# Performance work log

Measured on AMD Instinct MI355X. Metric: run time of the kernel, lower is better.

Reference implementation:

```python
import jax, jax.numpy as jnp
import numpy as np

MAX_N = 21
COORD = 3
TOTAL_T = 100
K_RANK = 3
POWER_STEPS = 10


def _recon_single(D, Wt, u_noise, x_noise):
    """D, Wt: [N,N]; u_noise: [K_RANK,N]; x_noise: [N,3]. Returns X: [N,3]."""
    N = MAX_N
    # dist_to_gram (classical MDS double-centering)
    D_row = jnp.sum(D, 0, keepdims=True) / N
    D_col = jnp.sum(D, 1, keepdims=True) / N
    D_mean = jnp.sum(D) / (N * N)
    B = -0.5 * (D - D_row - D_col + D_mean)
    # low_rank_approx_power: k=3 deflated power iterations, 10 steps each
    A = B
    us = []
    for i in range(K_RANK):
        u = u_noise[i]
        for _ in range(POWER_STEPS):
            # F.normalize(u, dim=0, p=2, eps=0.001)
            u = u / jnp.maximum(jnp.linalg.norm(u), 1e-3)
            u = A @ u
        eig_sq = jnp.sum(u * u)
        u = u / jnp.power(eig_sq + 0.01, 0.25)
        us.append(u)
        A = A - jnp.outer(u, u)
    X0 = jnp.stack(us, -1) + x_noise  # [N,3]

    T = jnp.float32(TOTAL_T)

    def energy(X):
        diff = X[None, :, :] - X[:, None, :]          # [N,N,3], D_X[i,j]=||X_j-X_i||^2
        D_X = jnp.sum(diff * diff, -1) + 0.01
        return jnp.sum(Wt * jnp.square(D - D_X))

    def step(X, t):
        g = jax.grad(energy)(X)
        dX = -0.1 * g
        speed = jnp.sqrt(jnp.sum(dX * dX, 1, keepdims=True) + 1e-3)
        alpha_t = 0.1 + (5.0 - 0.1) * ((T - t) / T)
        scale = alpha_t * jnp.tanh(speed / alpha_t) / speed
        return X + dX * scale, None

    X, _ = jax.lax.scan(step, X0, jnp.arange(TOTAL_T, dtype=jnp.float32))
    return X


def _forward(gnn_edge_out, W1, b1, W2, b2, u_noise, x_noise, batch_size):
    h_nf = W1.shape[1]
    # edge_mlp1 (MLP with 1 layer -> Linear + ReLU)
    edge_out = jax.nn.relu(gnn_edge_out @ W1 + b1)                     # [B*N*N, h]
    emb = jnp.sum(edge_out.reshape(batch_size, MAX_N, MAX_N, h_nf), axis=(1, 2))  # [B, h]
    # edge_mlp2 -> symmetrize -> softplus
    e2 = (edge_out @ W2 + b2).reshape(batch_size, MAX_N, MAX_N, 2)
    e2 = e2 + jnp.transpose(e2, (0, 2, 1, 3))
    dw = jax.nn.softplus(e2)
    D_init = dw[..., 0] * (1.0 - jnp.eye(MAX_N, dtype=dw.dtype))       # [B,N,N]
    W = dw[..., 1]                                                     # [B,N,N]
    X_pred = jax.vmap(_recon_single)(D_init, W, u_noise, x_noise)      # [B,N,3]
    return D_init, W, emb, X_pred


def setup_inputs() -> dict:
    key = jax.random.key(0)
    ks = jax.random.split(key, 5)
    B, h_nf = 1024, 256
    n_edges = B * MAX_N * MAX_N
    return {
        "gnn_edge_out": jax.random.normal(ks[0], (n_edges, h_nf), jnp.float32),
        "W1": jax.random.normal(ks[1], (h_nf, h_nf), jnp.float32) * (1.0 / np.sqrt(h_nf)),
        "b1": jnp.zeros((h_nf,), jnp.float32),
        "W2": jax.random.normal(ks[2], (h_nf, 2), jnp.float32) * (1.0 / np.sqrt(h_nf)),
        "b2": jnp.zeros((2,), jnp.float32),
        "u_noise": jax.random.normal(ks[3], (B, K_RANK, MAX_N), jnp.float32),
        "x_noise": jax.random.normal(ks[4], (B, MAX_N, COORD), jnp.float32),
        "batch_size": B,
    }


def reference(gnn_edge_out, W1, b1, W2, b2, u_noise, x_noise, batch_size):
    return _forward(gnn_edge_out, W1, b1, W2, b2, u_noise, x_noise, batch_size)
```

## Files before the change

kernel.cpp:

```cpp
#include <hip/hip_runtime.h>
#include <hip/hip_bf16.h>
#include <math.h>

#define B_SZ 1024
#define NMAX 21
#define NN 441
#define HNF 256
#define TOT_ROWS (B_SZ * NN)
#define TILES_PER_BATCH 7
#define BMV 63

typedef short short8 __attribute__((ext_vector_type(8)));
typedef float float4v __attribute__((ext_vector_type(4)));

__device__ __forceinline__ unsigned short f2bf(float x) {
    union { float f; unsigned int u; } v; v.f = x;
    unsigned int r = v.u + 0x7FFFu + ((v.u >> 16) & 1u);
    return (unsigned short)(r >> 16);
}

__device__ __forceinline__ unsigned pk_bf16(float lo, float hi) {
    __hip_bfloat162 h = __float22bfloat162_rn(float2{lo, hi});
    return *reinterpret_cast<unsigned*>(&h);
}

__device__ __forceinline__ float softplus_fast(float x) {
    float e = __builtin_amdgcn_exp2f(-fabsf(x) * 1.44269504088896f);
    float lg = __builtin_amdgcn_logf(1.f + e);
    return fmaxf(x, 0.f) + 0.69314718055995f * lg;
}

__device__ __forceinline__ float tanh_fast(float x) {
    float e = __builtin_amdgcn_exp2f(x * 2.8853900817779268f);
    float q = __builtin_amdgcn_rcpf(e + 1.f);
    return fmaf(-2.f, q, 1.f);
}

__global__ __launch_bounds__(256) void pack_w1(const float* __restrict__ W1,
                                               short* __restrict__ B0p,
                                               float* __restrict__ emb)
{
    int id = blockIdx.x * 256 + threadIdx.x;
    int j = id & 7, l = (id >> 3) & 63, f = (id >> 9) & 15, s = id >> 13;
    int k = s * 32 + ((l >> 4) << 3) + j;
    int c = (f << 4) + (l & 15);
    B0p[id] = (short)f2bf(W1[k * HNF + c]);
    #pragma unroll
    for (int e = 0; e < 4; e++)
        emb[(size_t)e * 65536 + id] = 0.f;
}

__global__ __launch_bounds__(512, 4) void fused_mlp_bf16(
    const float* __restrict__ gnn, const short* __restrict__ B0p,
    const float* __restrict__ b1, const float* __restrict__ W2,
    const float* __restrict__ b2,
    float* __restrict__ Dreg, float* __restrict__ Wreg, float* __restrict__ emb)
{
    __shared__ __align__(16) char ldsbuf[65536];
    float* stage = (float*)ldsbuf;
    short* Abf   = (short*)ldsbuf;
    __shared__ float red0[8][64];
    __shared__ float red1[8][64];

    const int t = threadIdx.x;
    const int w = t >> 6, l = t & 63;
    const int batch = blockIdx.x / TILES_PER_BATCH;
    const int tile  = blockIdx.x % TILES_PER_BATCH;
    const long row0 = (long)batch * NN + (long)tile * BMV;

    #pragma unroll
    for (int i = 0; i < 8; i++) {
        int r = (w << 3) + i;
        long ar = row0 + r;
        if (ar >= (long)TOT_ROWS) ar = TOT_ROWS - 1;
        const float* gsrc = gnn + ar * HNF + (l << 2);
        __builtin_amdgcn_global_load_lds(
            (const __attribute__((address_space(1))) unsigned*)gsrc,
            (__attribute__((address_space(3))) unsigned*)(stage + (r << 8)),
            16, 0, 0);
    }
    asm volatile("s_waitcnt vmcnt(0)" ::: "memory");

    const int kk_s = l >> 3;
    const int fk_s = (l >> 1) & 3;
    const int jh_s = l & 1;
    uint2 pv[8];
    #pragma unroll
    for (int i = 0; i < 8; i++) {
        int r = (w << 3) + i;
        float4 f = *(const float4*)(stage + (r << 8) + (l << 2));
        pv[i].x = pk_bf16(f.x, f.y);
        pv[i].y = pk_bf16(f.z, f.w);
    }
    __syncthreads();
    #pragma unroll
    for (int i = 0; i < 8; i++) {
        int r = (w << 3) + i;
        int di = (((kk_s << 2) + (r >> 4)) << 6) | (fk_s << 4) | (r & 15);
        *(uint2*)(Abf + (((size_t)(di ^ kk_s)) << 3) + (jh_s << 2)) = pv[i];
    }
    __syncthreads();

    const int frow = l & 15;
    const int fk   = l >> 4;

    float4v acc[4][2];
    #pragma unroll
    for (int m = 0; m < 4; m++)
        #pragma unroll
        for (int n = 0; n < 2; n++)
            acc[m][n] = (float4v){0.f, 0.f, 0.f, 0.f};

    #pragma unroll 2
    for (int kk = 0; kk < 8; ++kk) {
        short8 bf[2], af[4];
        #pragma unroll
        for (int n = 0; n < 2; n++) {
            int nf = (w << 1) + n;
            size_t off = (size_t)((((kk << 4) + nf) << 6) | l) << 3;
            bf[n] = *(const short8*)(B0p + off);
        }
        #pragma unroll
        for (int m = 0; m < 4; m++) {
            int di = ((((kk << 2) + m) << 6) | l) ^ kk;
            af[m] = *(const short8*)(Abf + (size_t)di * 8);
        }
        #pragma unroll
        for (int m = 0; m < 4; m++)
            #pragma unroll
            for (int n = 0; n < 2; n++)
                acc[m][n] = __builtin_amdgcn_mfma_f32_16x16x32_bf16(af[m], bf[n], acc[m][n], 0, 0, 0);
    }

    float w20[2], w21[2], b1v[2];
    #pragma unroll
    for (int n = 0; n < 2; n++) {
        int cc = (((w << 1) + n) << 4) + frow;
        b1v[n] = b1[cc];
        w20[n] = W2[2 * cc];
        w21[n] = W2[2 * cc + 1];
    }
    float ps0[4][4], ps1[4][4], embp[2] = {0.f, 0.f};
    #pragma unroll
    for (int m = 0; m < 4; m++)
        #pragma unroll
        for (int j = 0; j < 4; j++) { ps0[m][j] = 0.f; ps1[m][j] = 0.f; }

    #pragma unroll
    for (int m = 0; m < 4; m++)
        #pragma unroll
        for (int n = 0; n < 2; n++)
            #pragma unroll
            for (int j = 0; j < 4; j++) {
                float h = fmaxf(acc[m][n][j] + b1v[n], 0.f);
                ps0[m][j] += h * w20[n];
                ps1[m][j] += h * w21[n];
                int row = (m << 4) + (fk << 2) + j;
                if (row < BMV) embp[n] += h;
            }

    #pragma unroll
    for (int off = 1; off < 16; off <<= 1)
        #pragma unroll
        for (int m = 0; m < 4; m++)
            #pragma unroll
            for (int j = 0; j < 4; j++) {
                ps0[m][j] += __shfl_xor(ps0[m][j], off);
                ps1[m][j] += __shfl_xor(ps1[m][j], off);
            }
    if (frow == 0) {
        #pragma unroll
        for (int m = 0; m < 4; m++)
            #pragma unroll
            for (int j = 0; j < 4; j++) {
                int row = (m << 4) + (fk << 2) + j;
                red0[w][row] = ps0[m][j];
                red1[w][row] = ps1[m][j];
            }
    }

    #pragma unroll
    for (int n = 0; n < 2; n++) {
        embp[n] += __shfl_xor(embp[n], 16);
        embp[n] += __shfl_xor(embp[n], 32);
    }
    if (l < 16) {
        #pragma unroll
        for (int n = 0; n < 2; n++)
            atomicAdd(emb + (size_t)batch * 256 + (((w << 1) + n) << 4) + l, embp[n]);
    }

    __syncthreads();
    if (t < BMV) {
        float v0 = b2[0], v1 = b2[1];
        #pragma unroll
        for (int ww = 0; ww < 8; ww++) { v0 += red0[ww][t]; v1 += red1[ww][t]; }
        Dreg[row0 + t] = v0;
        Wreg[row0 + t] = v1;
    }
}

__global__ __launch_bounds__(64) void symrecon_kernel(
    float* __restrict__ Dreg, float* __restrict__ Wreg,
    const float* __restrict__ un, const float* __restrict__ xn,
    float* __restrict__ Xo)
{
    const int b = blockIdx.x, l = threadIdx.x;
    __shared__ float R0[NN], R1[NN];
    __shared__ float Rs[22], Us[22], Xs[3][22];

    float* Db = Dreg + (size_t)b * NN;
    float* Wb = Wreg + (size_t)b * NN;
    for (int idx = l; idx < NN; idx += 64) { R0[idx] = Db[idx]; R1[idx] = Wb[idx]; }
    if (l == 0) { Rs[21] = 0.f; Us[21] = 0.f; Xs[0][21] = 0.f; Xs[1][21] = 0.f; Xs[2][21] = 0.f; }
    __syncthreads();

    const int half = l >> 5;
    const int li   = l & 31;
    const bool act = li < NMAX;
    const int li0  = act ? li : 0;
    const int q0   = half * 11;

    float Drow[11], Wrow[11], WD[11];
    float rsh = 0.f;
    #pragma unroll
    for (int j = 0; j < 11; j++) {
        int q = q0 + j;
        bool v = act && (q < NMAX);
        int qc = v ? q : 0;
        float rd = R0[li0 * NMAX + qc] + R0[qc * NMAX + li0];
        float rw = R1[li0 * NMAX + qc] + R1[qc * NMAX + li0];
        float d  = (v && q != li) ? softplus_fast(rd) : 0.f;
        float wv = v ? softplus_fast(rw) : 0.f;
        Drow[j] = d; Wrow[j] = wv; WD[j] = wv * d;
        rsh += d;
    }
    if (act) {
        #pragma unroll
        for (int j = 0; j < 11; j++) {
            int q = q0 + j;
            if (q < NMAX) {
                Db[li * NMAX + q] = Drow[j];
                Wb[li * NMAX + q] = Wrow[j];
            }
        }
    }

    float rsf = rsh + __shfl_xor(rsh, 32);
    float tot = rsh;
    #pragma unroll
    for (int m = 1; m < 64; m <<= 1) tot += __shfl_xor(tot, m);
    const float mean = tot * (1.f / (float)NN);
    const float rsn  = rsf * (1.f / (float)NMAX);
    if (act && half == 0) Rs[li] = rsn;
    float Arow[11];
    #pragma unroll
    for (int j = 0; j < 11; j++) {
        int q = q0 + j;
        bool v = act && (q < NMAX);
        float rsq = Rs[q];
        Arow[j] = v ? -0.5f * (Drow[j] - rsn - rsq + mean) : 0.f;
    }

    float xc[3];
    #pragma unroll
    for (int e = 0; e < 3; e++) {
        float u = act ? un[(size_t)b * 63 + e * NMAX + li] : 0.f;
        for (int s = 0; s < 10; s++) {
            float n2 = (act && half == 0) ? u * u : 0.f;
            #pragma unroll
            for (int m = 1; m < 64; m <<= 1) n2 += __shfl_xor(n2, m);
            u *= fminf(__builtin_amdgcn_rsqf(n2), 1000.f);
            if (act && half == 0) Us[li] = u;
            float a = 0.f;
            #pragma unroll
            for (int j = 0; j < 11; j++) a = fmaf(Arow[j], Us[q0 + j], a);
            a += __shfl_xor(a, 32);
            u = act ? a : 0.f;
        }
        float e2 = (act && half == 0) ? u * u : 0.f;
        #pragma unroll
        for (int m = 1; m < 64; m <<= 1) e2 += __shfl_xor(e2, m);
        u *= sqrtf(__builtin_amdgcn_rsqf(e2 + 0.01f));
        xc[e] = u;
        if (act && half == 0) Us[li] = u;
        #pragma unroll
        for (int j = 0; j < 11; j++) Arow[j] = fmaf(-u, Us[q0 + j], Arow[j]);
    }
    float x = xc[0], y = xc[1], z = xc[2];
    if (act) {
        x += xn[(size_t)b * 63 + li * 3 + 0];
        y += xn[(size_t)b * 63 + li * 3 + 1];
        z += xn[(size_t)b * 63 + li * 3 + 2];
    }
    if (act && half == 0) { Xs[0][li] = x; Xs[1][li] = y; Xs[2][li] = z; }

    for (int tstep = 0; tstep < 100; tstep++) {
        float gx = 0.f, gy = 0.f, gz = 0.f;
        #pragma unroll
        for (int j = 0; j < 11; j++) {
            int q = q0 + j;
            float dx = x - Xs[0][q];
            float dy = y - Xs[1][q];
            float dz = z - Xs[2][q];
            float s  = fmaf(dx, dx, fmaf(dy, dy, fmaf(dz, dz, 0.01f)));
            float cm = fmaf(-Wrow[j], s, WD[j]);
            gx = fmaf(cm, dx, gx);
            gy = fmaf(cm, dy, gy);
            gz = fmaf(cm, dz, gz);
        }
        gx += __shfl_xor(gx, 32);
        gy += __shfl_xor(gy, 32);
        gz += __shfl_xor(gz, 32);
        float d0 = 0.8f * gx, d1 = 0.8f * gy, d2 = 0.8f * gz;
        float ss = fmaf(d0, d0, fmaf(d1, d1, fmaf(d2, d2, 1e-3f)));
        float inv_sp = __builtin_amdgcn_rsqf(ss);
        float speed  = ss * inv_sp;
        float alpha  = fmaf(-0.049f, (float)tstep, 5.0f);
        float th     = tanh_fast(speed * __builtin_amdgcn_rcpf(alpha));
        float scale  = alpha * th * inv_sp;
        x = fmaf(d0, scale, x);
        y = fmaf(d1, scale, y);
        z = fmaf(d2, scale, z);
        if (act && half == 0) { Xs[0][li] = x; Xs[1][li] = y; Xs[2][li] = z; }
    }
    if (act && half == 0) {
        Xo[(size_t)b * 63 + li * 3 + 0] = x;
        Xo[(size_t)b * 63 + li * 3 + 1] = y;
        Xo[(size_t)b * 63 + li * 3 + 2] = z;
    }
}

extern "C" void kernel_launch(void* const* d_in, const int* in_sizes, int n_in,
                              void* d_out, int out_size, void* d_ws, size_t ws_size,
                              hipStream_t stream) {
    const float* gnn = (const float*)d_in[0];
    const float* W1  = (const float*)d_in[1];
    const float* b1  = (const float*)d_in[2];
    const float* W2  = (const float*)d_in[3];
    const float* b2  = (const float*)d_in[4];
    const float* un  = (const float*)d_in[5];
    const float* xn  = (const float*)d_in[6];

    float* out  = (float*)d_out;
    float* Dreg = out;
    float* Wreg = out + (size_t)TOT_ROWS;
    float* emb  = out + (size_t)2 * TOT_ROWS;
    float* Xo   = out + (size_t)2 * TOT_ROWS + B_SZ*256;

    short* B0p = (short*)d_ws;

    pack_w1<<<dim3(256), dim3(256), 0, stream>>>(W1, B0p, emb);

    fused_mlp_bf16<<<dim3(B_SZ * TILES_PER_BATCH), dim3(512), 0, stream>>>(
        gnn, B0p, b1, W2, b2, Dreg, Wreg, emb);

    symrecon_kernel<<<dim3(B_SZ), dim3(64), 0, stream>>>(Dreg, Wreg, un, xn, Xo);
}
```

Before: 269.4 us.

## Shrink MLP tiles to 32 rows with 256 threads and split load wait

The fused MLP kernel now processes 32-row tiles (14 per batch) with 4 waves instead of 63-row tiles with 8 waves. Each wave computes 2x4 MFMA fragments instead of 4x2, and LDS use is halved. It also waits on half the global-to-LDS loads before converting them to bf16, overlapping conversion with the remaining loads. The intent is more resident blocks and better latency hiding, at the cost of twice the blocks, more emb atomics, and more redundant B-fragment loads per row.

After: 245.7 us. 1.1x faster.

```diff
diff --git a/kernel.cpp b/kernel.cpp
--- a/kernel.cpp
+++ b/kernel.cpp
@@ -7,8 +7,8 @@
 #define NN 441
 #define HNF 256
 #define TOT_ROWS (B_SZ * NN)
-#define TILES_PER_BATCH 7
-#define BMV 63
+#define TILES_PB 14
+#define TROWS 32
 
 typedef short short8 __attribute__((ext_vector_type(8)));
 typedef float float4v __attribute__((ext_vector_type(4)));
@@ -50,23 +50,24 @@
         emb[(size_t)e * 65536 + id] = 0.f;
 }
 
-__global__ __launch_bounds__(512, 4) void fused_mlp_bf16(
+__global__ __launch_bounds__(256, 4) void fused_mlp_bf16(
     const float* __restrict__ gnn, const short* __restrict__ B0p,
     const float* __restrict__ b1, const float* __restrict__ W2,
     const float* __restrict__ b2,
     float* __restrict__ Dreg, float* __restrict__ Wreg, float* __restrict__ emb)
 {
-    __shared__ __align__(16) char ldsbuf[65536];
+    __shared__ __align__(16) char ldsbuf[32768];
     float* stage = (float*)ldsbuf;
     short* Abf   = (short*)ldsbuf;
-    __shared__ float red0[8][64];
-    __shared__ float red1[8][64];
+    __shared__ float red0[4][32];
+    __shared__ float red1[4][32];
 
     const int t = threadIdx.x;
     const int w = t >> 6, l = t & 63;
-    const int batch = blockIdx.x / TILES_PER_BATCH;
-    const int tile  = blockIdx.x % TILES_PER_BATCH;
-    const long row0 = (long)batch * NN + (long)tile * BMV;
+    const int batch = blockIdx.x / TILES_PB;
+    const int tile  = blockIdx.x % TILES_PB;
+    const long row0 = (long)batch * NN + (long)tile * TROWS;
+    const int vr = (tile == TILES_PB - 1) ? (NN - (TILES_PB - 1) * TROWS) : TROWS;
 
     #pragma unroll
     for (int i = 0; i < 8; i++) {
@@ -79,90 +80,97 @@
             (__attribute__((address_space(3))) unsigned*)(stage + (r << 8)),
             16, 0, 0);
     }
+
+    uint2 pv[8];
+    asm volatile("s_waitcnt vmcnt(4)" ::: "memory");
+    #pragma unroll
+    for (int i = 0; i < 4; i++) {
+        float4 f = *(const float4*)(stage + (((w << 3) + i) << 8) + (l << 2));
+        pv[i].x = pk_bf16(f.x, f.y);
+        pv[i].y = pk_bf16(f.z, f.w);
+    }
     asm volatile("s_waitcnt vmcnt(0)" ::: "memory");
+    #pragma unroll
+    for (int i = 4; i < 8; i++) {
+        float4 f = *(const float4*)(stage + (((w << 3) + i) << 8) + (l << 2));
+        pv[i].x = pk_bf16(f.x, f.y);
+        pv[i].y = pk_bf16(f.z, f.w);
+    }
+    __syncthreads();
 
     const int kk_s = l >> 3;
     const int fk_s = (l >> 1) & 3;
     const int jh_s = l & 1;
-    uint2 pv[8];
     #pragma unroll
     for (int i = 0; i < 8; i++) {
         int r = (w << 3) + i;
-        float4 f = *(const float4*)(stage + (r << 8) + (l << 2));
-        pv[i].x = pk_bf16(f.x, f.y);
-        pv[i].y = pk_bf16(f.z, f.w);
-    }
-    __syncthreads();
-    #pragma unroll
-    for (int i = 0; i < 8; i++) {
-        int r = (w << 3) + i;
-        int di = (((kk_s << 2) + (r >> 4)) << 6) | (fk_s << 4) | (r & 15);
-        *(uint2*)(Abf + (((size_t)(di ^ kk_s)) << 3) + (jh_s << 2)) = pv[i];
+        int di = (((kk_s << 1) + (r >> 4)) << 6) | (fk_s << 4) | (r & 15);
+        *(uint2*)((char*)Abf + (((size_t)(di ^ kk_s)) << 4) + (jh_s << 3)) = pv[i];
     }
     __syncthreads();
 
     const int frow = l & 15;
     const int fk   = l >> 4;
 
-    float4v acc[4][2];
-    #pragma unroll
-    for (int m = 0; m < 4; m++)
-        #pragma unroll
-        for (int n = 0; n < 2; n++)
+    float4v acc[2][4];
+    #pragma unroll
+    for (int m = 0; m < 2; m++)
+        #pragma unroll
+        for (int n = 0; n < 4; n++)
             acc[m][n] = (float4v){0.f, 0.f, 0.f, 0.f};
 
     #pragma unroll 2
     for (int kk = 0; kk < 8; ++kk) {
-        short8 bf[2], af[4];
-        #pragma unroll
-        for (int n = 0; n < 2; n++) {
-            int nf = (w << 1) + n;
+        short8 bf[4], af[2];
+        #pragma unroll
+        for (int n = 0; n < 4; n++) {
+            int nf = (w << 2) + n;
             size_t off = (size_t)((((kk << 4) + nf) << 6) | l) << 3;
             bf[n] = *(const short8*)(B0p + off);
         }
         #pragma unroll
-        for (int m = 0; m < 4; m++) {
-            int di = ((((kk << 2) + m) << 6) | l) ^ kk;
+        for (int m = 0; m < 2; m++) {
+            int di = ((((kk << 1) + m) << 6) | l) ^ kk;
             af[m] = *(const short8*)(Abf + (size_t)di * 8);
         }
         #pragma unroll
-        for (int m = 0; m < 4; m++)
-            #pragma unroll
-            for (int n = 0; n < 2; n++)
+        for (int m = 0; m < 2; m++)
+            #pragma unroll
+            for (int n = 0; n < 4; n++)
                 acc[m][n] = __builtin_amdgcn_mfma_f32_16x16x32_bf16(af[m], bf[n], acc[m][n], 0, 0, 0);
     }
 
-    float w20[2], w21[2], b1v[2];
-    #pragma unroll
-    for (int n = 0; n < 2; n++) {
-        int cc = (((w << 1) + n) << 4) + frow;
+    float w20[4], w21[4], b1v[4];
+    #pragma unroll
+    for (int n = 0; n < 4; n++) {
+        int cc = (((w << 2) + n) << 4) + frow;
         b1v[n] = b1[cc];
         w20[n] = W2[2 * cc];
         w21[n] = W2[2 * cc + 1];
     }
-    float ps0[4][4], ps1[4][4], embp[2] = {0.f, 0.f};
-    #pragma unroll
-    for (int m = 0; m < 4; m++)
+    float ps0[2][4], ps1[2][4], embp[4] = {0.f, 0.f, 0.f, 0.f};
+    #pragma unroll
+    for (int m = 0; m < 2; m++)
         #pragma unroll
         for (int j = 0; j < 4; j++) { ps0[m][j] = 0.f; ps1[m][j] = 0.f; }
 
     #pragma unroll
-    for (int m = 0; m < 4; m++)
-        #pragma unroll
-        for (int n = 0; n < 2; n++)
+    for (int m = 0; m < 2; m++)
+        #pragma unroll
+        for (int n = 0; n < 4; n++)
             #pragma unroll
             for (int j = 0; j < 4; j++) {
                 float h = fmaxf(acc[m][n][j] + b1v[n], 0.f);
                 ps0[m][j] += h * w20[n];
                 ps1[m][j] += h * w21[n];
                 int row = (m << 4) + (fk << 2) + j;
-                if (row < BMV) embp[n] += h;
+                if (row < vr) embp[n] += h;
             }
 
     #pragma unroll
     for (int off = 1; off < 16; off <<= 1)
         #pragma unroll
-        for (int m = 0; m < 4; m++)
+        for (int m = 0; m < 2; m++)
             #pragma unroll
             for (int j = 0; j < 4; j++) {
                 ps0[m][j] += __shfl_xor(ps0[m][j], off);
@@ -170,7 +178,7 @@
             }
     if (frow == 0) {
         #pragma unroll
-        for (int m = 0; m < 4; m++)
+        for (int m = 0; m < 2; m++)
             #pragma unroll
             for (int j = 0; j < 4; j++) {
                 int row = (m << 4) + (fk << 2) + j;
@@ -180,21 +188,20 @@
     }
 
     #pragma unroll
-    for (int n = 0; n < 2; n++) {
+    for (int n = 0; n < 4; n++) {
         embp[n] += __shfl_xor(embp[n], 16);
         embp[n] += __shfl_xor(embp[n], 32);
     }
     if (l < 16) {
         #pragma unroll
-        for (int n = 0; n < 2; n++)
-            atomicAdd(emb + (size_t)batch * 256 + (((w << 1) + n) << 4) + l, embp[n]);
+        for (int n = 0; n < 4; n++)
+            atomicAdd(emb + (size_t)batch * 256 + (((w << 2) + n) << 4) + l, embp[n]);
     }
 
     __syncthreads();
-    if (t < BMV) {
-        float v0 = b2[0], v1 = b2[1];
-        #pragma unroll
-        for (int ww = 0; ww < 8; ww++) { v0 += red0[ww][t]; v1 += red1[ww][t]; }
+    if (t < vr) {
+        float v0 = b2[0] + red0[0][t] + red0[1][t] + red0[2][t] + red0[3][t];
+        float v1 = b2[1] + red1[0][t] + red1[1][t] + red1[2][t] + red1[3][t];
         Dreg[row0 + t] = v0;
         Wreg[row0 + t] = v1;
     }
@@ -352,7 +359,7 @@
 
     pack_w1<<<dim3(256), dim3(256), 0, stream>>>(W1, B0p, emb);
 
-    fused_mlp_bf16<<<dim3(B_SZ * TILES_PER_BATCH), dim3(512), 0, stream>>>(
+    fused_mlp_bf16<<<dim3(B_SZ * TILES_PB), dim3(256), 0, stream>>>(
         gnn, B0p, b1, W2, b2, Dreg, Wreg, emb);
 
     symrecon_kernel<<<dim3(B_SZ), dim3(64), 0, stream>>>(Dreg, Wreg, un, xn, Xo);
```
